# Optimization experiments

Measured on AMD Instinct MI355X. Metric: run time of the kernel, lower is better.

## Reference

```python
import jax, jax.numpy as jnp
import numpy as np

N, C_IN, C_OUT, M, K = 100000, 256, 512, 25000, 16
EPS = 1e-5

def setup_inputs() -> dict:
    key = jax.random.key(0)
    k1, k2, k3 = jax.random.split(key, 3)
    x = jax.random.normal(k1, (N, C_IN), dtype=jnp.float32)
    idx = jax.random.randint(k2, (M, K), 0, N)  # kNN neighbor indices from queryandgroup
    gamma = jnp.ones((C_IN,), dtype=jnp.float32)
    beta = jnp.zeros((C_IN,), dtype=jnp.float32)
    W = jax.random.normal(k3, (C_IN, C_OUT), dtype=jnp.float32) * (1.0 / np.sqrt(C_IN))
    b = jnp.zeros((C_OUT,), dtype=jnp.float32)
    return {"x": x, "idx": idx, "gamma": gamma, "beta": beta, "W": W, "b": b}

def reference(x, idx, gamma, beta, W, b):
    # queryandgroup: gather k neighbor features per downsampled point -> [M, K, C_IN]
    g = x[idx]
    # LayerNorm over channel dim
    mu = jnp.mean(g, axis=-1, keepdims=True)
    var = jnp.mean(jnp.square(g - mu), axis=-1, keepdims=True)
    g = (g - mu) * jax.lax.rsqrt(var + EPS) * gamma + beta
    # Linear: [M, K, C_IN] @ [C_IN, C_OUT] + b
    h = jnp.einsum('mki,io->mko', g, W) + b
    # GroupedMaxPool: max over the k neighbors -> [M, C_OUT]
    return jnp.max(h, axis=1)
```

## Files before the change

kernel.cpp:

```cpp
#include <hip/hip_runtime.h>

typedef _Float16 f16x8 __attribute__((ext_vector_type(8)));
typedef unsigned short ushort8 __attribute__((ext_vector_type(8)));
typedef float f32x4 __attribute__((ext_vector_type(4)));

#define C_IN     256
#define C_OUT    512
#define M_PTS    25000
#define KNN      16
#define P_BLK    4
#define ROWS     (P_BLK * KNN)
#define ROWB     528
#define NTHREADS 256

__device__ __forceinline__ unsigned short f2h(float f) {
    _Float16 h = (_Float16)f;
    return __builtin_bit_cast(unsigned short, h);
}

__global__ void pack_w_kernel(const float* __restrict__ W, unsigned short* __restrict__ Wp) {
    int t = blockIdx.x * blockDim.x + threadIdx.x;
    int j    = t & 7;
    int lane = (t >> 3) & 63;
    int kk   = (t >> 9) & 7;
    int nt   = t >> 12;
    int k = kk * 32 + ((lane >> 4) << 3) + j;
    int n = nt * 16 + (lane & 15);
    Wp[t] = f2h(W[k * C_OUT + n]);
}

__global__ __launch_bounds__(NTHREADS, 2)
void fused_gather_ln_gemm_max(const float* __restrict__ x,
                              const int* __restrict__ idx,
                              const float* __restrict__ gamma,
                              const float* __restrict__ beta,
                              const unsigned short* __restrict__ Wp,
                              const float* __restrict__ bias,
                              float* __restrict__ out) {
    __shared__ char Ab[ROWS * ROWB];

    const int tid  = threadIdx.x;
    const int lane = tid & 63;
    const int wave = tid >> 6;
    const int m0   = blockIdx.x * P_BLK;

    float gm[16], bt[16];
    const int cg = (tid & 15) * 16;
    #pragma unroll
    for (int q = 0; q < 4; ++q) {
        float4 g4 = ((const float4*)(gamma + cg))[q];
        float4 b4 = ((const float4*)(beta  + cg))[q];
        gm[4*q+0] = g4.x; gm[4*q+1] = g4.y; gm[4*q+2] = g4.z; gm[4*q+3] = g4.w;
        bt[4*q+0] = b4.x; bt[4*q+1] = b4.y; bt[4*q+2] = b4.z; bt[4*q+3] = b4.w;
    }
    #pragma unroll
    for (int it = 0; it < ROWS / 16; ++it) {
        const int r  = it * 16 + (tid >> 4);
        const int xr = idx[m0 * KNN + r];
        const float4* xp = (const float4*)(x + (size_t)xr * C_IN) + (tid & 15) * 4;
        float vv[16];
        float s = 0.f, sq = 0.f;
        #pragma unroll
        for (int q = 0; q < 4; ++q) {
            float4 v4 = xp[q];
            vv[4*q+0] = v4.x; vv[4*q+1] = v4.y; vv[4*q+2] = v4.z; vv[4*q+3] = v4.w;
        }
        #pragma unroll
        for (int e = 0; e < 16; ++e) { s += vv[e]; sq += vv[e]*vv[e]; }
        #pragma unroll
        for (int o = 1; o < 16; o <<= 1) {
            s  += __shfl_xor(s, o);
            sq += __shfl_xor(sq, o);
        }
        const float mu  = s * (1.0f/256.0f);
        const float var = sq * (1.0f/256.0f) - mu * mu;
        const float rs  = rsqrtf(var + 1e-5f);
        ushort8 c0, c1;
        #pragma unroll
        for (int e = 0; e < 8; ++e) c0[e] = f2h((vv[e]   - mu)*rs*gm[e]   + bt[e]);
        #pragma unroll
        for (int e = 0; e < 8; ++e) c1[e] = f2h((vv[e+8] - mu)*rs*gm[e+8] + bt[e+8]);
        const int cb = (tid & 15) * 32;
        *(ushort8*)(Ab + r*ROWB + cb)      = c0;
        *(ushort8*)(Ab + r*ROWB + cb + 16) = c1;
    }
    __syncthreads();

    #pragma unroll 1
    for (int ntp = 0; ntp < 4; ++ntp) {
        const int nt0 = wave * 8 + ntp * 2;
        const int nt1 = nt0 + 1;
        f16x8 b0[8], b1[8];
        #pragma unroll
        for (int kk = 0; kk < 8; ++kk) {
            b0[kk] = ((const f16x8*)Wp)[(nt0*8 + kk)*64 + lane];
            b1[kk] = ((const f16x8*)Wp)[(nt1*8 + kk)*64 + lane];
        }
        const float bias0 = bias[nt0*16 + (lane & 15)];
        const float bias1 = bias[nt1*16 + (lane & 15)];
        #pragma unroll 1
        for (int p = 0; p < P_BLK; ++p) {
            const int r = p*16 + (lane & 15);
            const int rowbase = r * ROWB;
            f32x4 acc0 = {0.f,0.f,0.f,0.f}, acc1 = {0.f,0.f,0.f,0.f};
            #pragma unroll
            for (int kk = 0; kk < 8; ++kk) {
                f16x8 a = *(const f16x8*)(Ab + rowbase + kk*64 + ((lane >> 4) << 4));
                acc0 = __builtin_amdgcn_mfma_f32_16x16x32_f16(a, b0[kk], acc0, 0, 0, 0);
                acc1 = __builtin_amdgcn_mfma_f32_16x16x32_f16(a, b1[kk], acc1, 0, 0, 0);
            }
            float v0 = fmaxf(fmaxf(acc0[0], acc0[1]), fmaxf(acc0[2], acc0[3]));
            float v1 = fmaxf(fmaxf(acc1[0], acc1[1]), fmaxf(acc1[2], acc1[3]));
            v0 = fmaxf(v0, __shfl_xor(v0, 16));
            v0 = fmaxf(v0, __shfl_xor(v0, 32));
            v1 = fmaxf(v1, __shfl_xor(v1, 16));
            v1 = fmaxf(v1, __shfl_xor(v1, 32));
            if (lane < 16) {
                out[(size_t)(m0 + p) * C_OUT + nt0*16 + lane] = v0 + bias0;
                out[(size_t)(m0 + p) * C_OUT + nt1*16 + lane] = v1 + bias1;
            }
        }
    }
}

extern "C" void kernel_launch(void* const* d_in, const int* in_sizes, int n_in,
                              void* d_out, int out_size, void* d_ws, size_t ws_size,
                              hipStream_t stream) {
    const float* x     = (const float*)d_in[0];
    const int*   idx   = (const int*)d_in[1];
    const float* gamma = (const float*)d_in[2];
    const float* beta  = (const float*)d_in[3];
    const float* W     = (const float*)d_in[4];
    const float* b     = (const float*)d_in[5];
    float* out = (float*)d_out;
    unsigned short* Wp = (unsigned short*)d_ws;

    hipLaunchKernelGGL(pack_w_kernel, dim3((C_IN * C_OUT) / 256), dim3(256), 0, stream, W, Wp);
    hipLaunchKernelGGL(fused_gather_ln_gemm_max, dim3(M_PTS / P_BLK), dim3(NTHREADS), 0, stream,
                       x, idx, gamma, beta, Wp, b, out);
}
```

Measured before the change: 152.8 us.

## Interleave all four point blocks in one k-loop with streamed W fragments

```diff
diff --git a/kernel.cpp b/kernel.cpp
--- a/kernel.cpp
+++ b/kernel.cpp
@@ -12,6 +12,8 @@
 #define ROWS     (P_BLK * KNN)
 #define ROWB     528
 #define NTHREADS 256
+
+#define MFMA16(a, b, c) __builtin_amdgcn_mfma_f32_16x16x32_f16(a, b, c, 0, 0, 0)
 
 __device__ __forceinline__ unsigned short f2h(float f) {
     _Float16 h = (_Float16)f;
@@ -86,39 +88,71 @@
     }
     __syncthreads();
 
+    const int rb0 = (0*16 + (lane & 15)) * ROWB;
+    const int rb1 = (1*16 + (lane & 15)) * ROWB;
+    const int rb2 = (2*16 + (lane & 15)) * ROWB;
+    const int rb3 = (3*16 + (lane & 15)) * ROWB;
+    const int csub = (lane >> 4) << 4;
+
     #pragma unroll 1
     for (int ntp = 0; ntp < 4; ++ntp) {
         const int nt0 = wave * 8 + ntp * 2;
         const int nt1 = nt0 + 1;
-        f16x8 b0[8], b1[8];
+        f32x4 a00 = {0.f,0.f,0.f,0.f}, a01 = {0.f,0.f,0.f,0.f};
+        f32x4 a10 = {0.f,0.f,0.f,0.f}, a11 = {0.f,0.f,0.f,0.f};
+        f32x4 a20 = {0.f,0.f,0.f,0.f}, a21 = {0.f,0.f,0.f,0.f};
+        f32x4 a30 = {0.f,0.f,0.f,0.f}, a31 = {0.f,0.f,0.f,0.f};
         #pragma unroll
         for (int kk = 0; kk < 8; ++kk) {
-            b0[kk] = ((const f16x8*)Wp)[(nt0*8 + kk)*64 + lane];
-            b1[kk] = ((const f16x8*)Wp)[(nt1*8 + kk)*64 + lane];
+            const f16x8 b0 = ((const f16x8*)Wp)[(nt0*8 + kk)*64 + lane];
+            const f16x8 b1 = ((const f16x8*)Wp)[(nt1*8 + kk)*64 + lane];
+            const int co = kk*64 + csub;
+            const f16x8 fa0 = *(const f16x8*)(Ab + rb0 + co);
+            const f16x8 fa1 = *(const f16x8*)(Ab + rb1 + co);
+            const f16x8 fa2 = *(const f16x8*)(Ab + rb2 + co);
+            const f16x8 fa3 = *(const f16x8*)(Ab + rb3 + co);
+            a00 = MFMA16(fa0, b0, a00);  a01 = MFMA16(fa0, b1, a01);
+            a10 = MFMA16(fa1, b0, a10);  a11 = MFMA16(fa1, b1, a11);
+            a20 = MFMA16(fa2, b0, a20);  a21 = MFMA16(fa2, b1, a21);
+            a30 = MFMA16(fa3, b0, a30);  a31 = MFMA16(fa3, b1, a31);
         }
         const float bias0 = bias[nt0*16 + (lane & 15)];
         const float bias1 = bias[nt1*16 + (lane & 15)];
-        #pragma unroll 1
-        for (int p = 0; p < P_BLK; ++p) {
-            const int r = p*16 + (lane & 15);
-            const int rowbase = r * ROWB;
-            f32x4 acc0 = {0.f,0.f,0.f,0.f}, acc1 = {0.f,0.f,0.f,0.f};
-            #pragma unroll
-            for (int kk = 0; kk < 8; ++kk) {
-                f16x8 a = *(const f16x8*)(Ab + rowbase + kk*64 + ((lane >> 4) << 4));
-                acc0 = __builtin_amdgcn_mfma_f32_16x16x32_f16(a, b0[kk], acc0, 0, 0, 0);
-                acc1 = __builtin_amdgcn_mfma_f32_16x16x32_f16(a, b1[kk], acc1, 0, 0, 0);
-            }
-            float v0 = fmaxf(fmaxf(acc0[0], acc0[1]), fmaxf(acc0[2], acc0[3]));
-            float v1 = fmaxf(fmaxf(acc1[0], acc1[1]), fmaxf(acc1[2], acc1[3]));
-            v0 = fmaxf(v0, __shfl_xor(v0, 16));
-            v0 = fmaxf(v0, __shfl_xor(v0, 32));
-            v1 = fmaxf(v1, __shfl_xor(v1, 16));
-            v1 = fmaxf(v1, __shfl_xor(v1, 32));
-            if (lane < 16) {
-                out[(size_t)(m0 + p) * C_OUT + nt0*16 + lane] = v0 + bias0;
-                out[(size_t)(m0 + p) * C_OUT + nt1*16 + lane] = v1 + bias1;
-            }
+        const int oc0 = nt0*16 + lane;
+        const int oc1 = nt1*16 + lane;
+
+        float v0, v1;
+        v0 = fmaxf(fmaxf(a00[0], a00[1]), fmaxf(a00[2], a00[3]));
+        v1 = fmaxf(fmaxf(a01[0], a01[1]), fmaxf(a01[2], a01[3]));
+        v0 = fmaxf(v0, __shfl_xor(v0, 16)); v0 = fmaxf(v0, __shfl_xor(v0, 32));
+        v1 = fmaxf(v1, __shfl_xor(v1, 16)); v1 = fmaxf(v1, __shfl_xor(v1, 32));
+        if (lane < 16) {
+            out[(size_t)(m0 + 0) * C_OUT + oc0] = v0 + bias0;
+            out[(size_t)(m0 + 0) * C_OUT + oc1] = v1 + bias1;
+        }
+        v0 = fmaxf(fmaxf(a10[0], a10[1]), fmaxf(a10[2], a10[3]));
+        v1 = fmaxf(fmaxf(a11[0], a11[1]), fmaxf(a11[2], a11[3]));
+        v0 = fmaxf(v0, __shfl_xor(v0, 16)); v0 = fmaxf(v0, __shfl_xor(v0, 32));
+        v1 = fmaxf(v1, __shfl_xor(v1, 16)); v1 = fmaxf(v1, __shfl_xor(v1, 32));
+        if (lane < 16) {
+            out[(size_t)(m0 + 1) * C_OUT + oc0] = v0 + bias0;
+            out[(size_t)(m0 + 1) * C_OUT + oc1] = v1 + bias1;
+        }
+        v0 = fmaxf(fmaxf(a20[0], a20[1]), fmaxf(a20[2], a20[3]));
+        v1 = fmaxf(fmaxf(a21[0], a21[1]), fmaxf(a21[2], a21[3]));
+        v0 = fmaxf(v0, __shfl_xor(v0, 16)); v0 = fmaxf(v0, __shfl_xor(v0, 32));
+        v1 = fmaxf(v1, __shfl_xor(v1, 16)); v1 = fmaxf(v1, __shfl_xor(v1, 32));
+        if (lane < 16) {
+            out[(size_t)(m0 + 2) * C_OUT + oc0] = v0 + bias0;
+            out[(size_t)(m0 + 2) * C_OUT + oc1] = v1 + bias1;
+        }
+        v0 = fmaxf(fmaxf(a30[0], a30[1]), fmaxf(a30[2], a30[3]));
+        v1 = fmaxf(fmaxf(a31[0], a31[1]), fmaxf(a31[2], a31[3]));
+        v0 = fmaxf(v0, __shfl_xor(v0, 16)); v0 = fmaxf(v0, __shfl_xor(v0, 32));
+        v1 = fmaxf(v1, __shfl_xor(v1, 16)); v1 = fmaxf(v1, __shfl_xor(v1, 32));
+        if (lane < 16) {
+            out[(size_t)(m0 + 3) * C_OUT + oc0] = v0 + bias0;
+            out[(size_t)(m0 + 3) * C_OUT + oc1] = v1 + bias1;
         }
     }
 }
```

Result: slower. 188.3 us (+23.3%).

## Assign each wave one point with A fragments in registers, stream all W tiles

Applied to the files above, without the earlier changes.

```diff
diff --git a/kernel.cpp b/kernel.cpp
--- a/kernel.cpp
+++ b/kernel.cpp
@@ -12,6 +12,8 @@
 #define ROWS     (P_BLK * KNN)
 #define ROWB     528
 #define NTHREADS 256
+
+#define MFMA16(a, b, c) __builtin_amdgcn_mfma_f32_16x16x32_f16(a, b, c, 0, 0, 0)
 
 __device__ __forceinline__ unsigned short f2h(float f) {
     _Float16 h = (_Float16)f;
@@ -86,39 +88,38 @@
     }
     __syncthreads();
 
+    const int rb   = (wave * 16 + (lane & 15)) * ROWB;
+    const int csub = (lane >> 4) << 4;
+
+    const f16x8 af0 = *(const f16x8*)(Ab + rb + 0*64 + csub);
+    const f16x8 af1 = *(const f16x8*)(Ab + rb + 1*64 + csub);
+    const f16x8 af2 = *(const f16x8*)(Ab + rb + 2*64 + csub);
+    const f16x8 af3 = *(const f16x8*)(Ab + rb + 3*64 + csub);
+    const f16x8 af4 = *(const f16x8*)(Ab + rb + 4*64 + csub);
+    const f16x8 af5 = *(const f16x8*)(Ab + rb + 5*64 + csub);
+    const f16x8 af6 = *(const f16x8*)(Ab + rb + 6*64 + csub);
+    const f16x8 af7 = *(const f16x8*)(Ab + rb + 7*64 + csub);
+
+    float* orow = out + (size_t)(m0 + wave) * C_OUT;
+
     #pragma unroll 1
-    for (int ntp = 0; ntp < 4; ++ntp) {
-        const int nt0 = wave * 8 + ntp * 2;
-        const int nt1 = nt0 + 1;
-        f16x8 b0[8], b1[8];
-        #pragma unroll
-        for (int kk = 0; kk < 8; ++kk) {
-            b0[kk] = ((const f16x8*)Wp)[(nt0*8 + kk)*64 + lane];
-            b1[kk] = ((const f16x8*)Wp)[(nt1*8 + kk)*64 + lane];
-        }
-        const float bias0 = bias[nt0*16 + (lane & 15)];
-        const float bias1 = bias[nt1*16 + (lane & 15)];
-        #pragma unroll 1
-        for (int p = 0; p < P_BLK; ++p) {
-            const int r = p*16 + (lane & 15);
-            const int rowbase = r * ROWB;
-            f32x4 acc0 = {0.f,0.f,0.f,0.f}, acc1 = {0.f,0.f,0.f,0.f};
-            #pragma unroll
-            for (int kk = 0; kk < 8; ++kk) {
-                f16x8 a = *(const f16x8*)(Ab + rowbase + kk*64 + ((lane >> 4) << 4));
-                acc0 = __builtin_amdgcn_mfma_f32_16x16x32_f16(a, b0[kk], acc0, 0, 0, 0);
-                acc1 = __builtin_amdgcn_mfma_f32_16x16x32_f16(a, b1[kk], acc1, 0, 0, 0);
-            }
-            float v0 = fmaxf(fmaxf(acc0[0], acc0[1]), fmaxf(acc0[2], acc0[3]));
-            float v1 = fmaxf(fmaxf(acc1[0], acc1[1]), fmaxf(acc1[2], acc1[3]));
-            v0 = fmaxf(v0, __shfl_xor(v0, 16));
-            v0 = fmaxf(v0, __shfl_xor(v0, 32));
-            v1 = fmaxf(v1, __shfl_xor(v1, 16));
-            v1 = fmaxf(v1, __shfl_xor(v1, 32));
-            if (lane < 16) {
-                out[(size_t)(m0 + p) * C_OUT + nt0*16 + lane] = v0 + bias0;
-                out[(size_t)(m0 + p) * C_OUT + nt1*16 + lane] = v1 + bias1;
-            }
+    for (int nt = 0; nt < 32; ++nt) {
+        const f16x8* Bp = (const f16x8*)Wp + (size_t)(nt * 8) * 64 + lane;
+        f32x4 acc = {0.f, 0.f, 0.f, 0.f};
+        const f16x8 b0 = Bp[0*64];  acc = MFMA16(af0, b0, acc);
+        const f16x8 b1 = Bp[1*64];  acc = MFMA16(af1, b1, acc);
+        const f16x8 b2 = Bp[2*64];  acc = MFMA16(af2, b2, acc);
+        const f16x8 b3 = Bp[3*64];  acc = MFMA16(af3, b3, acc);
+        const f16x8 b4 = Bp[4*64];  acc = MFMA16(af4, b4, acc);
+        const f16x8 b5 = Bp[5*64];  acc = MFMA16(af5, b5, acc);
+        const f16x8 b6 = Bp[6*64];  acc = MFMA16(af6, b6, acc);
+        const f16x8 b7 = Bp[7*64];  acc = MFMA16(af7, b7, acc);
+
+        float v = fmaxf(fmaxf(acc[0], acc[1]), fmaxf(acc[2], acc[3]));
+        v = fmaxf(v, __shfl_xor(v, 16));
+        v = fmaxf(v, __shfl_xor(v, 32));
+        if (lane < 16) {
+            orow[nt*16 + lane] = v + bias[nt*16 + lane];
         }
     }
 }
```

Result: slower. 274.2 us (+79.5%).
